# Optimization experiments

Hardware: AMD Instinct MI355X
Metric: run time of the kernel (lower is better)

Reference implementation:

```python
import jax, jax.numpy as jnp
import numpy as np

B, NOBJ = 64, 16
NUM_CLASSES = 91
IOU_TH = 0.5
NEG_POS = 3
VAR0, VAR1 = 0.1, 0.2
IMG = 300.0


def _ssd300_priors():
    # Standard SSD300 PriorBox: 8732 priors in center-size form (cx, cy, w, h), normalized to [0,1]
    fmaps = [38, 19, 10, 5, 3, 1]
    steps = [8, 16, 32, 64, 100, 300]
    min_s = [30, 60, 111, 162, 213, 264]
    max_s = [60, 111, 162, 213, 264, 315]
    ars = [[2], [2, 3], [2, 3], [2, 3], [2], [2]]
    out = []
    for k, f in enumerate(fmaps):
        for i in range(f):
            for j in range(f):
                cx = (j + 0.5) * steps[k] / IMG
                cy = (i + 0.5) * steps[k] / IMG
                s = min_s[k] / IMG
                out.append([cx, cy, s, s])
                sp = float(np.sqrt(s * max_s[k] / IMG))
                out.append([cx, cy, sp, sp])
                for ar in ars[k]:
                    r = float(np.sqrt(ar))
                    out.append([cx, cy, s * r, s / r])
                    out.append([cx, cy, s / r, s * r])
    return np.clip(np.asarray(out, np.float32), 0.0, 1.0)


def setup_inputs() -> dict:
    priors = jnp.asarray(_ssd300_priors())  # [8732, 4]
    P = priors.shape[0]
    key = jax.random.key(0)
    k1, k2, k3, k4, k5 = jax.random.split(key, 5)
    loc_data = jax.random.normal(k1, (B, P, 4), jnp.float32)
    conf_data = jax.random.normal(k2, (B, P, NUM_CLASSES), jnp.float32)
    centers = jax.random.uniform(k3, (B, NOBJ, 2), minval=40.0, maxval=260.0)
    half = jax.random.uniform(k5, (B, NOBJ, 2), minval=10.0, maxval=40.0)
    gt_boxes = jnp.concatenate([centers - half, centers + half], axis=-1)  # point form, pixel coords
    gt_labels = jax.random.randint(k4, (B, NOBJ), 1, NUM_CLASSES).astype(jnp.int32)
    return {"loc_data": loc_data, "conf_data": conf_data, "gt_boxes": gt_boxes,
            "gt_labels": gt_labels, "priors": priors}


def _point_form(pr):
    return jnp.concatenate([pr[:, :2] - pr[:, 2:] / 2, pr[:, :2] + pr[:, 2:] / 2], axis=1)


def _jaccard(boxes, pboxes):
    # boxes [N,4], pboxes [P,4] both point form -> IoU [N,P]
    lt = jnp.maximum(boxes[:, None, :2], pboxes[None, :, :2])
    rb = jnp.minimum(boxes[:, None, 2:], pboxes[None, :, 2:])
    wh = jnp.clip(rb - lt, 0.0)
    inter = wh[..., 0] * wh[..., 1]
    area_a = ((boxes[:, 2] - boxes[:, 0]) * (boxes[:, 3] - boxes[:, 1]))[:, None]
    area_b = ((pboxes[:, 2] - pboxes[:, 0]) * (pboxes[:, 3] - pboxes[:, 1]))[None, :]
    return inter / (area_a + area_b - inter)


def _encode(matched, priors):
    # matched [P,4] point form, priors [P,4] center-size form
    g_cxcy = ((matched[:, :2] + matched[:, 2:]) / 2 - priors[:, :2]) / (VAR0 * priors[:, 2:])
    g_wh = jnp.log((matched[:, 2:] - matched[:, :2]) / priors[:, 2:]) / VAR1
    return jnp.concatenate([g_cxcy, g_wh], axis=1)


def _match(boxes, labels, priors):
    # boxes [NOBJ,4] normalized point form; labels [NOBJ]; priors [P,4]
    ov = _jaccard(boxes, _point_form(priors))            # [NOBJ, P]
    best_prior_idx = jnp.argmax(ov, axis=1)              # [NOBJ]
    best_truth_ov = jnp.max(ov, axis=0)                  # [P]
    best_truth_idx = jnp.argmax(ov, axis=0)              # [P]
    best_truth_ov = best_truth_ov.at[best_prior_idx].set(2.0)
    for j in range(NOBJ):  # small fixed loop, matches torch in-order scatter
        best_truth_idx = best_truth_idx.at[best_prior_idx[j]].set(j)
    matched = boxes[best_truth_idx]                      # [P,4]
    conf = labels[best_truth_idx]
    conf = jnp.where(best_truth_ov < IOU_TH, 0, conf)
    return _encode(matched, priors), conf


def reference(loc_data, conf_data, gt_boxes, gt_labels, priors):
    P = priors.shape[0]
    loc_t, conf_t = jax.vmap(lambda b, l: _match(b / IMG, l, priors))(gt_boxes, gt_labels)
    pos = conf_t > 0                                      # [B,P]
    # localization loss: SmoothL1 (beta=1), summed over positives
    diff = loc_data - loc_t
    ad = jnp.abs(diff)
    sl1 = jnp.where(ad < 1.0, 0.5 * diff * diff, ad - 0.5)
    loss_l = jnp.sum(sl1 * pos[..., None].astype(sl1.dtype))
    # hard negative mining on per-prior CE loss
    lse = jax.nn.logsumexp(conf_data, axis=-1)            # [B,P]
    gathered = jnp.take_along_axis(conf_data, conf_t[..., None].astype(jnp.int32), axis=-1)[..., 0]
    ce_all = lse - gathered                                # [B,P]
    mine = jnp.where(pos, 0.0, ce_all)
    order = jnp.argsort(-mine, axis=1)
    rank = jnp.argsort(order, axis=1)
    num_pos = jnp.sum(pos, axis=1, keepdims=True)
    num_neg = jnp.clip(NEG_POS * num_pos, 1, P - 1)
    neg = rank < num_neg
    mask = pos | neg
    loss_c = jnp.sum(ce_all * mask.astype(ce_all.dtype))
    N = jnp.maximum(jnp.sum(num_pos).astype(jnp.float32), 1.0)
    return jnp.stack([loss_l / N, loss_c / N])  # [loss_l, loss_c]
```

## Files before the change

kernel.cpp:

```cpp
#include <hip/hip_runtime.h>
#include <math.h>

#define BATCH 64
#define NOBJ 16
#define NPRIOR 8732
#define NC 91
#define IMG 300.0f
#define GPB 1092
#define NGROUP (GPB * BATCH)
#define CE_GRID 6144
#define GBINS 2048
#define MSPLIT 16
#define SL 546

__global__ __launch_bounds__(256) void k_match1(
    const float* __restrict__ loc_data,
    const float* __restrict__ gt_boxes,
    const int*   __restrict__ gt_labels,
    const float* __restrict__ priors,
    int*   __restrict__ conf_t,
    float* __restrict__ ll_part,
    int*   __restrict__ np_part,
    float* __restrict__ candv,
    int*   __restrict__ candi)
{
    __shared__ float bx0[NOBJ], by0[NOBJ], bx1[NOBJ], by1[NOBJ], barea[NOBJ];
    __shared__ int   blab[NOBJ];
    __shared__ float rv[NOBJ][4];
    __shared__ int   ri[NOBJ][4];
    __shared__ float red_f[4];
    __shared__ int   red_i[4];

    const int b    = blockIdx.y;
    const int blk  = blockIdx.x;
    const int tid  = threadIdx.x;
    const int lane = tid & 63;
    const int wave = tid >> 6;
    const int p0   = blk * SL;
    const int pend = min(p0 + SL, NPRIOR);

    if (tid < NOBJ) {
        float4 g = ((const float4*)gt_boxes)[(size_t)b * NOBJ + tid];
        float x0 = g.x * (1.0f / IMG), y0 = g.y * (1.0f / IMG);
        float x1 = g.z * (1.0f / IMG), y1 = g.w * (1.0f / IMG);
        bx0[tid] = x0; by0[tid] = y0; bx1[tid] = x1; by1[tid] = y1;
        barea[tid] = (x1 - x0) * (y1 - y0);
        blab[tid] = gt_labels[b * NOBJ + tid];
    }
    __syncthreads();

    float bv[NOBJ];
    int   bi[NOBJ];
#pragma unroll
    for (int j = 0; j < NOBJ; j++) { bv[j] = -1.0f; bi[j] = 0x7fffffff; }

    int np_local = 0;
    float ll_local = 0.0f;

    for (int p = p0 + tid; p < pend; p += 256) {
        float4 pr = ((const float4*)priors)[p];
        float cx = pr.x, cy = pr.y, w = pr.z, h = pr.w;
        float px0 = cx - 0.5f * w, py0 = cy - 0.5f * h;
        float px1 = cx + 0.5f * w, py1 = cy + 0.5f * h;
        float pa = w * h;
        float maxv = -1.0f; int maxj = 0;
#pragma unroll
        for (int j = 0; j < NOBJ; j++) {
            float ltx = fmaxf(bx0[j], px0), lty = fmaxf(by0[j], py0);
            float rbx = fminf(bx1[j], px1), rby = fminf(by1[j], py1);
            float iw = fmaxf(rbx - ltx, 0.0f), ih = fmaxf(rby - lty, 0.0f);
            float inter = iw * ih;
            float iou = inter / (barea[j] + pa - inter);
            if (iou > maxv) { maxv = iou; maxj = j; }
            if (iou > bv[j]) { bv[j] = iou; bi[j] = p; }
        }
        int conf = (maxv < 0.5f) ? 0 : blab[maxj];
        conf_t[(size_t)b * NPRIOR + p] = conf;
        if (conf > 0) {
            np_local++;
            float mx0 = bx0[maxj], my0 = by0[maxj];
            float mx1 = bx1[maxj], my1 = by1[maxj];
            float g0 = ((mx0 + mx1) * 0.5f - cx) / (0.1f * w);
            float g1 = ((my0 + my1) * 0.5f - cy) / (0.1f * h);
            float g2 = logf((mx1 - mx0) / w) * 5.0f;
            float g3 = logf((my1 - my0) / h) * 5.0f;
            float4 lv = ((const float4*)loc_data)[(size_t)b * NPRIOR + p];
            float d0 = lv.x - g0, d1 = lv.y - g1, d2 = lv.z - g2, d3 = lv.w - g3;
            float a0 = fabsf(d0), a1 = fabsf(d1), a2 = fabsf(d2), a3 = fabsf(d3);
            ll_local += (a0 < 1.f ? 0.5f * d0 * d0 : a0 - 0.5f)
                      + (a1 < 1.f ? 0.5f * d1 * d1 : a1 - 0.5f)
                      + (a2 < 1.f ? 0.5f * d2 * d2 : a2 - 0.5f)
                      + (a3 < 1.f ? 0.5f * d3 * d3 : a3 - 0.5f);
        }
    }

#pragma unroll
    for (int j = 0; j < NOBJ; j++) {
        float v = bv[j]; int ix = bi[j];
        for (int off = 32; off; off >>= 1) {
            float v2 = __shfl_xor(v, off);
            int   i2 = __shfl_xor(ix, off);
            if (v2 > v || (v2 == v && i2 < ix)) { v = v2; ix = i2; }
        }
        if (lane == 0) { rv[j][wave] = v; ri[j][wave] = ix; }
    }
    for (int off = 32; off; off >>= 1) {
        ll_local += __shfl_xor(ll_local, off);
        np_local += __shfl_xor(np_local, off);
    }
    if (lane == 0) { red_f[wave] = ll_local; red_i[wave] = np_local; }
    __syncthreads();
    if (tid < NOBJ) {
        int j = tid;
        float v = rv[j][0]; int ix = ri[j][0];
#pragma unroll
        for (int w2 = 1; w2 < 4; w2++) {
            float v2 = rv[j][w2]; int i2 = ri[j][w2];
            if (v2 > v || (v2 == v && i2 < ix)) { v = v2; ix = i2; }
        }
        size_t o = ((size_t)b * MSPLIT + blk) * NOBJ + j;
        candv[o] = v;
        candi[o] = ix;
    }
    if (tid == 0) {
        ll_part[b * MSPLIT + blk] = red_f[0] + red_f[1] + red_f[2] + red_f[3];
        np_part[b * MSPLIT + blk] = red_i[0] + red_i[1] + red_i[2] + red_i[3];
    }
}

__global__ __launch_bounds__(64) void k_bpi_fix(
    const float* __restrict__ loc_data,
    const float* __restrict__ gt_boxes,
    const int*   __restrict__ gt_labels,
    const float* __restrict__ priors,
    const float* __restrict__ candv,
    const int*   __restrict__ candi,
    int*   __restrict__ conf_t,
    float* __restrict__ ll_fix,
    int*   __restrict__ np_fix)
{
    __shared__ int bpi_s[NOBJ];
    const int b = blockIdx.x;
    const int lane = threadIdx.x;

    if (lane < NOBJ) {
        size_t base = (size_t)b * MSPLIT * NOBJ + lane;
        float v = candv[base]; int ix = candi[base];
#pragma unroll
        for (int c = 1; c < MSPLIT; c++) {
            float v2 = candv[base + c * NOBJ];
            int   i2 = candi[base + c * NOBJ];
            if (v2 > v || (v2 == v && i2 < ix)) { v = v2; ix = i2; }
        }
        bpi_s[lane] = ix;
    }
    __syncthreads();

    float ll_d = 0.0f;
    int   np_d = 0;

    if (lane < NOBJ) {
        const int j = lane;
        const int ps = bpi_s[j];
        bool last = true;
        for (int j2 = j + 1; j2 < NOBJ; j2++)
            if (bpi_s[j2] == ps) last = false;
        if (last) {
            float4 pr = ((const float4*)priors)[ps];
            float cx = pr.x, cy = pr.y, w = pr.z, h = pr.w;
            float px0 = cx - 0.5f * w, py0 = cy - 0.5f * h;
            float px1 = cx + 0.5f * w, py1 = cy + 0.5f * h;
            float pa = w * h;
            float maxv = -1.0f;
            float mx0 = 0, my0 = 0, mx1 = 0, my1 = 0;
            float jx0 = 0, jy0 = 0, jx1 = 0, jy1 = 0;
            for (int j2 = 0; j2 < NOBJ; j2++) {
                float4 g = ((const float4*)gt_boxes)[(size_t)b * NOBJ + j2];
                float x0 = g.x * (1.0f / IMG), y0 = g.y * (1.0f / IMG);
                float x1 = g.z * (1.0f / IMG), y1 = g.w * (1.0f / IMG);
                float area = (x1 - x0) * (y1 - y0);
                float ltx = fmaxf(x0, px0), lty = fmaxf(y0, py0);
                float rbx = fminf(x1, px1), rby = fminf(y1, py1);
                float iw = fmaxf(rbx - ltx, 0.0f), ih = fmaxf(rby - lty, 0.0f);
                float inter = iw * ih;
                float iou = inter / (area + pa - inter);
                if (iou > maxv) { maxv = iou; mx0 = x0; my0 = y0; mx1 = x1; my1 = y1; }
                if (j2 == j)    { jx0 = x0; jy0 = y0; jx1 = x1; jy1 = y1; }
            }
            float4 lv = ((const float4*)loc_data)[(size_t)b * NPRIOR + ps];
            if (maxv >= 0.5f) {
                float g0 = ((mx0 + mx1) * 0.5f - cx) / (0.1f * w);
                float g1 = ((my0 + my1) * 0.5f - cy) / (0.1f * h);
                float g2 = logf((mx1 - mx0) / w) * 5.0f;
                float g3 = logf((my1 - my0) / h) * 5.0f;
                float d0 = lv.x - g0, d1 = lv.y - g1, d2 = lv.z - g2, d3 = lv.w - g3;
                float a0 = fabsf(d0), a1 = fabsf(d1), a2 = fabsf(d2), a3 = fabsf(d3);
                ll_d -= (a0 < 1.f ? 0.5f * d0 * d0 : a0 - 0.5f)
                      + (a1 < 1.f ? 0.5f * d1 * d1 : a1 - 0.5f)
                      + (a2 < 1.f ? 0.5f * d2 * d2 : a2 - 0.5f)
                      + (a3 < 1.f ? 0.5f * d3 * d3 : a3 - 0.5f);
                np_d -= 1;
            }
            {
                float g0 = ((jx0 + jx1) * 0.5f - cx) / (0.1f * w);
                float g1 = ((jy0 + jy1) * 0.5f - cy) / (0.1f * h);
                float g2 = logf((jx1 - jx0) / w) * 5.0f;
                float g3 = logf((jy1 - jy0) / h) * 5.0f;
                float d0 = lv.x - g0, d1 = lv.y - g1, d2 = lv.z - g2, d3 = lv.w - g3;
                float a0 = fabsf(d0), a1 = fabsf(d1), a2 = fabsf(d2), a3 = fabsf(d3);
                ll_d += (a0 < 1.f ? 0.5f * d0 * d0 : a0 - 0.5f)
                      + (a1 < 1.f ? 0.5f * d1 * d1 : a1 - 0.5f)
                      + (a2 < 1.f ? 0.5f * d2 * d2 : a2 - 0.5f)
                      + (a3 < 1.f ? 0.5f * d3 * d3 : a3 - 0.5f);
                np_d += 1;
            }
            conf_t[(size_t)b * NPRIOR + ps] = gt_labels[b * NOBJ + j];
        }
    }

    for (int off = 32; off; off >>= 1) {
        ll_d += __shfl_xor(ll_d, off);
        np_d += __shfl_xor(np_d, off);
    }
    if (lane == 0) { ll_fix[b] = ll_d; np_fix[b] = np_d; }
}

#define CE_ISSUE(gg, R0, R1, R2, NF)                                           \
    {   int b_ = (gg) / GPB, ci_ = (gg) - b_ * GPB;                            \
        int p0_ = ci_ * 8;                                                     \
        int rows_ = min(8, NPRIOR - p0_);                                      \
        NF = (rows_ * NC) >> 2;                                                \
        const float4* s_ = (const float4*)(conf_data + ((size_t)b_ * NPRIOR + p0_) * NC); \
        R0 = s_[tid];                                                          \
        if (tid + 64  < NF) R1 = s_[tid + 64];                                 \
        if (tid + 128 < NF) R2 = s_[tid + 128]; }

#define CT_LOAD(gg)                                                            \
    ( conf_t[(size_t)((gg) / GPB) * NPRIOR + ((gg) - ((gg) / GPB) * GPB) * 8 + (tid >> 3)] )

#define CE_WRITE(BUF, R0, R1, R2, NF)                                          \
    {   float4* d_ = (float4*)sbuf[BUF];                                       \
        d_[tid] = R0;                                                          \
        if (tid + 64  < NF) d_[tid + 64]  = R1;                                \
        if (tid + 128 < NF) d_[tid + 128] = R2; }

#define CE_COMPUTE(gg, BUF, TG)                                                \
    {   int b_ = (gg) / GPB, ci_ = (gg) - b_ * GPB;                            \
        int p0_ = ci_ * 8;                                                     \
        int rows_ = min(8, NPRIOR - p0_);                                      \
        int rr_ = tid >> 3, q_ = tid & 7;                                      \
        if (rr_ < rows_) {                                                     \
            const float* row_ = sbuf[BUF] + rr_ * NC;                          \
            float s_ = 0.0f;                                                   \
            _Pragma("unroll")                                                  \
            for (int i_ = q_; i_ < NC; i_ += 8) s_ += __expf(row_[i_]);        \
            s_ += __shfl_xor(s_, 1);                                           \
            s_ += __shfl_xor(s_, 2);                                           \
            s_ += __shfl_xor(s_, 4);                                           \
            if (q_ == 0) {                                                     \
                size_t o_ = (size_t)b_ * NPRIOR + p0_ + rr_;                   \
                int tgt_ = TG;                                                 \
                float ce_ = __logf(s_) - row_[tgt_];                           \
                if (tgt_ > 0) { pos_acc += ce_; mine[o_] = 0.0f; }             \
                else          { mine[o_] = fmaxf(ce_, 0.0f); }                 \
            } } }

__global__ __launch_bounds__(64) void k_ce(
    const float* __restrict__ conf_data,
    const int*   __restrict__ conf_t,
    float* __restrict__ mine,
    float* __restrict__ lc_part)
{
    __shared__ float sbuf[2][8 * NC];
    const int tid = threadIdx.x;
    const int G = CE_GRID;

    float4 a0, a1, a2, b0, b1, b2;
    int nfA = 0, nfB = 0;
    float pos_acc = 0.0f;

    int g = blockIdx.x;
    CE_ISSUE(g, a0, a1, a2, nfA);
    int tcur = CT_LOAD(g);
    if (g + G < NGROUP) CE_ISSUE(g + G, b0, b1, b2, nfB);
    CE_WRITE(0, a0, a1, a2, nfA);

    for (; g < NGROUP; g += 2 * G) {
        int tnext = (g + G < NGROUP) ? CT_LOAD(g + G) : 0;
        if (g + 2 * G < NGROUP) CE_ISSUE(g + 2 * G, a0, a1, a2, nfA);
        CE_COMPUTE(g, 0, tcur);
        if (g + G < NGROUP) {
            CE_WRITE(1, b0, b1, b2, nfB);
            int tn2 = (g + 2 * G < NGROUP) ? CT_LOAD(g + 2 * G) : 0;
            if (g + 3 * G < NGROUP) CE_ISSUE(g + 3 * G, b0, b1, b2, nfB);
            CE_COMPUTE(g + G, 1, tnext);
            if (g + 2 * G < NGROUP) CE_WRITE(0, a0, a1, a2, nfA);
            tcur = tn2;
        }
    }

    for (int off = 32; off; off >>= 1) pos_acc += __shfl_xor(pos_acc, off);
    if (tid == 0) lc_part[blockIdx.x] = pos_acc;
}

__global__ __launch_bounds__(256) void k_histsel(
    const float* __restrict__ mine,
    const int*   __restrict__ np_part,
    const int*   __restrict__ np_fix,
    float* __restrict__ lc2)
{
    __shared__ int   lh[GBINS];
    __shared__ float ls[GBINS];
    __shared__ int   wtot[4];
    __shared__ int   s_B0, s_r;
    __shared__ float red_f[4];

    const int b = blockIdx.x;
    const int tid = threadIdx.x;
    const int lane = tid & 63;
    const int wave = tid >> 6;

#pragma unroll
    for (int j = 0; j < GBINS / 256; j++) {
        lh[tid + j * 256] = 0;
        ls[tid + j * 256] = 0.0f;
    }
    __syncthreads();

    for (int i = tid; i < NPRIOR; i += 256) {
        float v = mine[(size_t)b * NPRIOR + i];
        int bin = min((int)(v * 128.0f), GBINS - 1);
        atomicAdd(&lh[bin], 1);
        atomicAdd(&ls[bin], v);
    }

    int np = np_fix[b];
#pragma unroll
    for (int c = 0; c < MSPLIT; c++) np += np_part[b * MSPLIT + c];
    const int kk = min(max(3 * np, 1), NPRIOR - 1);
    __syncthreads();

    int   cnt[8];
    float sm[8];
#pragma unroll
    for (int j = 0; j < 8; j++) { cnt[j] = lh[tid * 8 + j]; sm[j] = ls[tid * 8 + j]; }
    int own = 0;
#pragma unroll
    for (int j = 0; j < 8; j++) own += cnt[j];

    int incl = own;
#pragma unroll
    for (int off = 1; off < 64; off <<= 1) {
        int t = __shfl_down(incl, off);
        incl += (lane + off < 64) ? t : 0;
    }
    if (lane == 0) wtot[wave] = incl;
    __syncthreads();
    int hi = 0;
#pragma unroll
    for (int w = 0; w < 4; w++) if (w > wave) hi += wtot[w];
    const int suf = (incl - own) + hi;

    int found = -1;
    int s2 = suf;
#pragma unroll
    for (int j = 7; j >= 0; j--) {
        if (found < 0 && s2 < kk && kk <= s2 + cnt[j])
            found = (tid * 8 + j) * 16384 + (kk - s2);
        s2 += cnt[j];
    }
    if (found >= 0) { s_B0 = found >> 14; s_r = found & 16383; }
    __syncthreads();
    const int B0 = s_B0;
    const int r  = s_r;

    float sg = 0.0f;
#pragma unroll
    for (int j = 0; j < 8; j++) {
        int bin = tid * 8 + j;
        if (bin > B0)       sg += sm[j];
        else if (bin == B0) sg += (float)r * (sm[j] / (float)cnt[j]);
    }
    for (int off = 32; off; off >>= 1) sg += __shfl_xor(sg, off);
    if (lane == 0) red_f[wave] = sg;
    __syncthreads();
    if (tid == 0) lc2[b] = red_f[0] + red_f[1] + red_f[2] + red_f[3];
}

__global__ __launch_bounds__(1024) void k_final(
    const float* __restrict__ lc_part, const float* __restrict__ lc2,
    const float* __restrict__ ll_part, const int* __restrict__ np_part,
    const float* __restrict__ ll_fix, const int* __restrict__ np_fix,
    float* __restrict__ out)
{
    __shared__ float rf[16][2];
    __shared__ int   rn[16];
    const int tid = threadIdx.x;
    float lc = 0.0f;
    for (int i = tid; i < CE_GRID; i += 1024) lc += lc_part[i];
    float ll = 0.0f; int np = 0;
    if (tid < BATCH) { lc += lc2[tid]; ll += ll_fix[tid]; np += np_fix[tid]; }
    if (tid < BATCH * MSPLIT) { ll += ll_part[tid]; np += np_part[tid]; }
    for (int off = 32; off; off >>= 1) {
        lc += __shfl_xor(lc, off);
        ll += __shfl_xor(ll, off);
        np += __shfl_xor(np, off);
    }
    const int lane = tid & 63, wave = tid >> 6;
    if (lane == 0) { rf[wave][0] = lc; rf[wave][1] = ll; rn[wave] = np; }
    __syncthreads();
    if (tid == 0) {
        float lcT = 0.0f, llT = 0.0f; int npT = 0;
        for (int w = 0; w < 16; w++) { lcT += rf[w][0]; llT += rf[w][1]; npT += rn[w]; }
        float N = fmaxf((float)npT, 1.0f);
        out[0] = llT / N;
        out[1] = lcT / N;
    }
}

extern "C" void kernel_launch(void* const* d_in, const int* in_sizes, int n_in,
                              void* d_out, int out_size, void* d_ws, size_t ws_size,
                              hipStream_t stream)
{
    const float* loc_data  = (const float*)d_in[0];
    const float* conf_data = (const float*)d_in[1];
    const float* gt_boxes  = (const float*)d_in[2];
    const int*   gt_labels = (const int*)d_in[3];
    const float* priors    = (const float*)d_in[4];
    float* out = (float*)d_out;

    char* ws = (char*)d_ws;
    float* ll_part  = (float*)(ws + 0);
    int*   np_part  = (int*)(ws + 4096);
    float* lc2      = (float*)(ws + 8192);
    float* ll_fix   = (float*)(ws + 8704);
    int*   np_fix   = (int*)(ws + 9216);
    float* lc_part  = (float*)(ws + 12288);
    int*   conf_t   = (int*)(ws + 65536);
    float* mine     = (float*)(ws + 65536 + 2235392);
    float* candv    = (float*)(ws + 7340032);
    int*   candi    = (int*)(ws + 7405568);

    hipLaunchKernelGGL(k_match1, dim3(MSPLIT, BATCH), dim3(256), 0, stream,
                       loc_data, gt_boxes, gt_labels, priors,
                       conf_t, ll_part, np_part, candv, candi);
    hipLaunchKernelGGL(k_bpi_fix, dim3(BATCH), dim3(64), 0, stream,
                       loc_data, gt_boxes, gt_labels, priors, candv, candi,
                       conf_t, ll_fix, np_fix);
    hipLaunchKernelGGL(k_ce, dim3(CE_GRID), dim3(64), 0, stream,
                       conf_data, conf_t, mine, lc_part);
    hipLaunchKernelGGL(k_histsel, dim3(BATCH), dim3(256), 0, stream,
                       mine, np_part, np_fix, lc2);
    hipLaunchKernelGGL(k_final, dim3(1), dim3(1024), 0, stream,
                       lc_part, lc2, ll_part, np_part, ll_fix, np_fix, out);
}
```

Before: 101.2 us.

## Fuse matching and logsumexp into one heterogeneous kernel, defer CE gather to histsel

The matching blocks and the conf_data logsumexp streaming now share one launch: 2 of every 5 blocks do prior matching and 3 run four independent double-buffered LSE waves. The LSE no longer depends on conf_t, so it runs concurrently with matching instead of after the bpi fix. The per-prior CE target gather and the positive-loss sum move into the histogram kernel, which reads lse and the class-0 logit and does a scattered load from conf_data for positives. This removes the serialization between matching and the large conf_data read, at the cost of extra lse/c0 buffers and a slower, more irregular histogram pass.

```diff
diff --git a/kernel.cpp b/kernel.cpp
--- a/kernel.cpp
+++ b/kernel.cpp
@@ -8,22 +8,61 @@
 #define IMG 300.0f
 #define GPB 1092
 #define NGROUP (GPB * BATCH)
-#define CE_GRID 6144
+#define LSE_WAVES 6144
 #define GBINS 2048
 #define MSPLIT 16
 #define SL 546
 
-__global__ __launch_bounds__(256) void k_match1(
+#define LSE_ISSUE(gg, R0, R1, R2, NF)                                          \
+    {   int b_ = (gg) / GPB, ci_ = (gg) - b_ * GPB;                            \
+        int p0_ = ci_ * 8;                                                     \
+        int rows_ = min(8, NPRIOR - p0_);                                      \
+        NF = (rows_ * NC) >> 2;                                                \
+        const float4* s_ = (const float4*)(conf_data + ((size_t)b_ * NPRIOR + p0_) * NC); \
+        R0 = s_[lane];                                                         \
+        if (lane + 64  < NF) R1 = s_[lane + 64];                               \
+        if (lane + 128 < NF) R2 = s_[lane + 128]; }
+
+#define LSE_WRITE(SB, R0, R1, R2, NF)                                          \
+    {   float4* d_ = (float4*)(SB);                                            \
+        d_[lane] = R0;                                                         \
+        if (lane + 64  < NF) d_[lane + 64]  = R1;                              \
+        if (lane + 128 < NF) d_[lane + 128] = R2; }
+
+#define LSE_COMPUTE(gg, SB)                                                    \
+    {   int b_ = (gg) / GPB, ci_ = (gg) - b_ * GPB;                            \
+        int p0_ = ci_ * 8;                                                     \
+        int rows_ = min(8, NPRIOR - p0_);                                      \
+        int rr_ = lane >> 3, q_ = lane & 7;                                    \
+        if (rr_ < rows_) {                                                     \
+            const float* row_ = (SB) + rr_ * NC;                               \
+            float s_ = 0.0f;                                                   \
+            _Pragma("unroll")                                                  \
+            for (int i_ = q_; i_ < NC; i_ += 8) s_ += __expf(row_[i_]);        \
+            s_ += __shfl_xor(s_, 1);                                           \
+            s_ += __shfl_xor(s_, 2);                                           \
+            s_ += __shfl_xor(s_, 4);                                           \
+            if (q_ == 0) {                                                     \
+                size_t o_ = (size_t)b_ * NPRIOR + p0_ + rr_;                   \
+                lse_g[o_] = __logf(s_);                                        \
+                c0_g[o_]  = row_[0];                                           \
+            } } }
+
+__global__ __launch_bounds__(256) void k_fused(
     const float* __restrict__ loc_data,
     const float* __restrict__ gt_boxes,
     const int*   __restrict__ gt_labels,
     const float* __restrict__ priors,
+    const float* __restrict__ conf_data,
     int*   __restrict__ conf_t,
     float* __restrict__ ll_part,
     int*   __restrict__ np_part,
     float* __restrict__ candv,
-    int*   __restrict__ candi)
+    int*   __restrict__ candi,
+    float* __restrict__ lse_g,
+    float* __restrict__ c0_g)
 {
+    __shared__ float sbuf[4][2][8 * NC];
     __shared__ float bx0[NOBJ], by0[NOBJ], bx1[NOBJ], by1[NOBJ], barea[NOBJ];
     __shared__ int   blab[NOBJ];
     __shared__ float rv[NOBJ][4];
@@ -31,100 +70,130 @@
     __shared__ float red_f[4];
     __shared__ int   red_i[4];
 
-    const int b    = blockIdx.y;
-    const int blk  = blockIdx.x;
+    const int bid  = blockIdx.x;
     const int tid  = threadIdx.x;
     const int lane = tid & 63;
-    const int wave = tid >> 6;
-    const int p0   = blk * SL;
-    const int pend = min(p0 + SL, NPRIOR);
-
-    if (tid < NOBJ) {
-        float4 g = ((const float4*)gt_boxes)[(size_t)b * NOBJ + tid];
-        float x0 = g.x * (1.0f / IMG), y0 = g.y * (1.0f / IMG);
-        float x1 = g.z * (1.0f / IMG), y1 = g.w * (1.0f / IMG);
-        bx0[tid] = x0; by0[tid] = y0; bx1[tid] = x1; by1[tid] = y1;
-        barea[tid] = (x1 - x0) * (y1 - y0);
-        blab[tid] = gt_labels[b * NOBJ + tid];
-    }
-    __syncthreads();
-
-    float bv[NOBJ];
-    int   bi[NOBJ];
-#pragma unroll
-    for (int j = 0; j < NOBJ; j++) { bv[j] = -1.0f; bi[j] = 0x7fffffff; }
-
-    int np_local = 0;
-    float ll_local = 0.0f;
-
-    for (int p = p0 + tid; p < pend; p += 256) {
-        float4 pr = ((const float4*)priors)[p];
-        float cx = pr.x, cy = pr.y, w = pr.z, h = pr.w;
-        float px0 = cx - 0.5f * w, py0 = cy - 0.5f * h;
-        float px1 = cx + 0.5f * w, py1 = cy + 0.5f * h;
-        float pa = w * h;
-        float maxv = -1.0f; int maxj = 0;
+    const int wv   = tid >> 6;
+    const int r5   = bid % 5;
+
+    if (r5 < 2) {
+        const int m   = (bid / 5) * 2 + r5;
+        const int blk = m % MSPLIT;
+        const int b   = m / MSPLIT;
+        const int p0   = blk * SL;
+        const int pend = min(p0 + SL, NPRIOR);
+
+        if (tid < NOBJ) {
+            float4 g = ((const float4*)gt_boxes)[(size_t)b * NOBJ + tid];
+            float x0 = g.x * (1.0f / IMG), y0 = g.y * (1.0f / IMG);
+            float x1 = g.z * (1.0f / IMG), y1 = g.w * (1.0f / IMG);
+            bx0[tid] = x0; by0[tid] = y0; bx1[tid] = x1; by1[tid] = y1;
+            barea[tid] = (x1 - x0) * (y1 - y0);
+            blab[tid] = gt_labels[b * NOBJ + tid];
+        }
+        __syncthreads();
+
+        float bv[NOBJ];
+        int   bi[NOBJ];
+#pragma unroll
+        for (int j = 0; j < NOBJ; j++) { bv[j] = -1.0f; bi[j] = 0x7fffffff; }
+
+        int np_local = 0;
+        float ll_local = 0.0f;
+
+        for (int p = p0 + tid; p < pend; p += 256) {
+            float4 pr = ((const float4*)priors)[p];
+            float cx = pr.x, cy = pr.y, w = pr.z, h = pr.w;
+            float px0 = cx - 0.5f * w, py0 = cy - 0.5f * h;
+            float px1 = cx + 0.5f * w, py1 = cy + 0.5f * h;
+            float pa = w * h;
+            float maxv = -1.0f; int maxj = 0;
+#pragma unroll
+            for (int j = 0; j < NOBJ; j++) {
+                float ltx = fmaxf(bx0[j], px0), lty = fmaxf(by0[j], py0);
+                float rbx = fminf(bx1[j], px1), rby = fminf(by1[j], py1);
+                float iw = fmaxf(rbx - ltx, 0.0f), ih = fmaxf(rby - lty, 0.0f);
+                float inter = iw * ih;
+                float iou = inter / (barea[j] + pa - inter);
+                if (iou > maxv) { maxv = iou; maxj = j; }
+                if (iou > bv[j]) { bv[j] = iou; bi[j] = p; }
+            }
+            int conf = (maxv < 0.5f) ? 0 : blab[maxj];
+            conf_t[(size_t)b * NPRIOR + p] = conf;
+            if (conf > 0) {
+                np_local++;
+                float mx0 = bx0[maxj], my0 = by0[maxj];
+                float mx1 = bx1[maxj], my1 = by1[maxj];
+                float g0 = ((mx0 + mx1) * 0.5f - cx) / (0.1f * w);
+                float g1 = ((my0 + my1) * 0.5f - cy) / (0.1f * h);
+                float g2 = logf((mx1 - mx0) / w) * 5.0f;
+                float g3 = logf((my1 - my0) / h) * 5.0f;
+                float4 lv = ((const float4*)loc_data)[(size_t)b * NPRIOR + p];
+                float d0 = lv.x - g0, d1 = lv.y - g1, d2 = lv.z - g2, d3 = lv.w - g3;
+                float a0 = fabsf(d0), a1 = fabsf(d1), a2 = fabsf(d2), a3 = fabsf(d3);
+                ll_local += (a0 < 1.f ? 0.5f * d0 * d0 : a0 - 0.5f)
+                          + (a1 < 1.f ? 0.5f * d1 * d1 : a1 - 0.5f)
+                          + (a2 < 1.f ? 0.5f * d2 * d2 : a2 - 0.5f)
+                          + (a3 < 1.f ? 0.5f * d3 * d3 : a3 - 0.5f);
+            }
+        }
+
 #pragma unroll
         for (int j = 0; j < NOBJ; j++) {
-            float ltx = fmaxf(bx0[j], px0), lty = fmaxf(by0[j], py0);
-            float rbx = fminf(bx1[j], px1), rby = fminf(by1[j], py1);
-            float iw = fmaxf(rbx - ltx, 0.0f), ih = fmaxf(rby - lty, 0.0f);
-            float inter = iw * ih;
-            float iou = inter / (barea[j] + pa - inter);
-            if (iou > maxv) { maxv = iou; maxj = j; }
-            if (iou > bv[j]) { bv[j] = iou; bi[j] = p; }
-        }
-        int conf = (maxv < 0.5f) ? 0 : blab[maxj];
-        conf_t[(size_t)b * NPRIOR + p] = conf;
-        if (conf > 0) {
-            np_local++;
-            float mx0 = bx0[maxj], my0 = by0[maxj];
-            float mx1 = bx1[maxj], my1 = by1[maxj];
-            float g0 = ((mx0 + mx1) * 0.5f - cx) / (0.1f * w);
-            float g1 = ((my0 + my1) * 0.5f - cy) / (0.1f * h);
-            float g2 = logf((mx1 - mx0) / w) * 5.0f;
-            float g3 = logf((my1 - my0) / h) * 5.0f;
-            float4 lv = ((const float4*)loc_data)[(size_t)b * NPRIOR + p];
-            float d0 = lv.x - g0, d1 = lv.y - g1, d2 = lv.z - g2, d3 = lv.w - g3;
-            float a0 = fabsf(d0), a1 = fabsf(d1), a2 = fabsf(d2), a3 = fabsf(d3);
-            ll_local += (a0 < 1.f ? 0.5f * d0 * d0 : a0 - 0.5f)
-                      + (a1 < 1.f ? 0.5f * d1 * d1 : a1 - 0.5f)
-                      + (a2 < 1.f ? 0.5f * d2 * d2 : a2 - 0.5f)
-                      + (a3 < 1.f ? 0.5f * d3 * d3 : a3 - 0.5f);
-        }
-    }
-
-#pragma unroll
-    for (int j = 0; j < NOBJ; j++) {
-        float v = bv[j]; int ix = bi[j];
+            float v = bv[j]; int ix = bi[j];
+            for (int off = 32; off; off >>= 1) {
+                float v2 = __shfl_xor(v, off);
+                int   i2 = __shfl_xor(ix, off);
+                if (v2 > v || (v2 == v && i2 < ix)) { v = v2; ix = i2; }
+            }
+            if (lane == 0) { rv[j][wv] = v; ri[j][wv] = ix; }
+        }
         for (int off = 32; off; off >>= 1) {
-            float v2 = __shfl_xor(v, off);
-            int   i2 = __shfl_xor(ix, off);
-            if (v2 > v || (v2 == v && i2 < ix)) { v = v2; ix = i2; }
-        }
-        if (lane == 0) { rv[j][wave] = v; ri[j][wave] = ix; }
-    }
-    for (int off = 32; off; off >>= 1) {
-        ll_local += __shfl_xor(ll_local, off);
-        np_local += __shfl_xor(np_local, off);
-    }
-    if (lane == 0) { red_f[wave] = ll_local; red_i[wave] = np_local; }
-    __syncthreads();
-    if (tid < NOBJ) {
-        int j = tid;
-        float v = rv[j][0]; int ix = ri[j][0];
-#pragma unroll
-        for (int w2 = 1; w2 < 4; w2++) {
-            float v2 = rv[j][w2]; int i2 = ri[j][w2];
-            if (v2 > v || (v2 == v && i2 < ix)) { v = v2; ix = i2; }
-        }
-        size_t o = ((size_t)b * MSPLIT + blk) * NOBJ + j;
-        candv[o] = v;
-        candi[o] = ix;
-    }
-    if (tid == 0) {
-        ll_part[b * MSPLIT + blk] = red_f[0] + red_f[1] + red_f[2] + red_f[3];
-        np_part[b * MSPLIT + blk] = red_i[0] + red_i[1] + red_i[2] + red_i[3];
+            ll_local += __shfl_xor(ll_local, off);
+            np_local += __shfl_xor(np_local, off);
+        }
+        if (lane == 0) { red_f[wv] = ll_local; red_i[wv] = np_local; }
+        __syncthreads();
+        if (tid < NOBJ) {
+            int j = tid;
+            float v = rv[j][0]; int ix = ri[j][0];
+#pragma unroll
+            for (int w2 = 1; w2 < 4; w2++) {
+                float v2 = rv[j][w2]; int i2 = ri[j][w2];
+                if (v2 > v || (v2 == v && i2 < ix)) { v = v2; ix = i2; }
+            }
+            size_t o = ((size_t)b * MSPLIT + blk) * NOBJ + j;
+            candv[o] = v;
+            candi[o] = ix;
+        }
+        if (tid == 0) {
+            ll_part[b * MSPLIT + blk] = red_f[0] + red_f[1] + red_f[2] + red_f[3];
+            np_part[b * MSPLIT + blk] = red_i[0] + red_i[1] + red_i[2] + red_i[3];
+        }
+    } else {
+        const int lblk = (bid / 5) * 3 + (r5 - 2);
+        int g = lblk * 4 + wv;
+        const int G = LSE_WAVES;
+        float* SB0 = &sbuf[wv][0][0];
+        float* SB1 = &sbuf[wv][1][0];
+
+        float4 a0, a1, a2, b0, b1, b2;
+        int nfA = 0, nfB = 0;
+
+        LSE_ISSUE(g, a0, a1, a2, nfA);
+        if (g + G < NGROUP) LSE_ISSUE(g + G, b0, b1, b2, nfB);
+        LSE_WRITE(SB0, a0, a1, a2, nfA);
+
+        for (; g < NGROUP; g += 2 * G) {
+            if (g + 2 * G < NGROUP) LSE_ISSUE(g + 2 * G, a0, a1, a2, nfA);
+            LSE_COMPUTE(g, SB0);
+            if (g + G < NGROUP) {
+                LSE_WRITE(SB1, b0, b1, b2, nfB);
+                if (g + 3 * G < NGROUP) LSE_ISSUE(g + 3 * G, b0, b1, b2, nfB);
+                LSE_COMPUTE(g + G, SB1);
+                if (g + 2 * G < NGROUP) LSE_WRITE(SB0, a0, a1, a2, nfA);
+            }
+        }
     }
 }
 
@@ -225,95 +294,22 @@
     if (lane == 0) { ll_fix[b] = ll_d; np_fix[b] = np_d; }
 }
 
-#define CE_ISSUE(gg, R0, R1, R2, NF)                                           \
-    {   int b_ = (gg) / GPB, ci_ = (gg) - b_ * GPB;                            \
-        int p0_ = ci_ * 8;                                                     \
-        int rows_ = min(8, NPRIOR - p0_);                                      \
-        NF = (rows_ * NC) >> 2;                                                \
-        const float4* s_ = (const float4*)(conf_data + ((size_t)b_ * NPRIOR + p0_) * NC); \
-        R0 = s_[tid];                                                          \
-        if (tid + 64  < NF) R1 = s_[tid + 64];                                 \
-        if (tid + 128 < NF) R2 = s_[tid + 128]; }
-
-#define CT_LOAD(gg)                                                            \
-    ( conf_t[(size_t)((gg) / GPB) * NPRIOR + ((gg) - ((gg) / GPB) * GPB) * 8 + (tid >> 3)] )
-
-#define CE_WRITE(BUF, R0, R1, R2, NF)                                          \
-    {   float4* d_ = (float4*)sbuf[BUF];                                       \
-        d_[tid] = R0;                                                          \
-        if (tid + 64  < NF) d_[tid + 64]  = R1;                                \
-        if (tid + 128 < NF) d_[tid + 128] = R2; }
-
-#define CE_COMPUTE(gg, BUF, TG)                                                \
-    {   int b_ = (gg) / GPB, ci_ = (gg) - b_ * GPB;                            \
-        int p0_ = ci_ * 8;                                                     \
-        int rows_ = min(8, NPRIOR - p0_);                                      \
-        int rr_ = tid >> 3, q_ = tid & 7;                                      \
-        if (rr_ < rows_) {                                                     \
-            const float* row_ = sbuf[BUF] + rr_ * NC;                          \
-            float s_ = 0.0f;                                                   \
-            _Pragma("unroll")                                                  \
-            for (int i_ = q_; i_ < NC; i_ += 8) s_ += __expf(row_[i_]);        \
-            s_ += __shfl_xor(s_, 1);                                           \
-            s_ += __shfl_xor(s_, 2);                                           \
-            s_ += __shfl_xor(s_, 4);                                           \
-            if (q_ == 0) {                                                     \
-                size_t o_ = (size_t)b_ * NPRIOR + p0_ + rr_;                   \
-                int tgt_ = TG;                                                 \
-                float ce_ = __logf(s_) - row_[tgt_];                           \
-                if (tgt_ > 0) { pos_acc += ce_; mine[o_] = 0.0f; }             \
-                else          { mine[o_] = fmaxf(ce_, 0.0f); }                 \
-            } } }
-
-__global__ __launch_bounds__(64) void k_ce(
+__global__ __launch_bounds__(256) void k_histsel2(
     const float* __restrict__ conf_data,
+    const float* __restrict__ lse_g,
+    const float* __restrict__ c0_g,
     const int*   __restrict__ conf_t,
-    float* __restrict__ mine,
-    float* __restrict__ lc_part)
-{
-    __shared__ float sbuf[2][8 * NC];
-    const int tid = threadIdx.x;
-    const int G = CE_GRID;
-
-    float4 a0, a1, a2, b0, b1, b2;
-    int nfA = 0, nfB = 0;
-    float pos_acc = 0.0f;
-
-    int g = blockIdx.x;
-    CE_ISSUE(g, a0, a1, a2, nfA);
-    int tcur = CT_LOAD(g);
-    if (g + G < NGROUP) CE_ISSUE(g + G, b0, b1, b2, nfB);
-    CE_WRITE(0, a0, a1, a2, nfA);
-
-    for (; g < NGROUP; g += 2 * G) {
-        int tnext = (g + G < NGROUP) ? CT_LOAD(g + G) : 0;
-        if (g + 2 * G < NGROUP) CE_ISSUE(g + 2 * G, a0, a1, a2, nfA);
-        CE_COMPUTE(g, 0, tcur);
-        if (g + G < NGROUP) {
-            CE_WRITE(1, b0, b1, b2, nfB);
-            int tn2 = (g + 2 * G < NGROUP) ? CT_LOAD(g + 2 * G) : 0;
-            if (g + 3 * G < NGROUP) CE_ISSUE(g + 3 * G, b0, b1, b2, nfB);
-            CE_COMPUTE(g + G, 1, tnext);
-            if (g + 2 * G < NGROUP) CE_WRITE(0, a0, a1, a2, nfA);
-            tcur = tn2;
-        }
-    }
-
-    for (int off = 32; off; off >>= 1) pos_acc += __shfl_xor(pos_acc, off);
-    if (tid == 0) lc_part[blockIdx.x] = pos_acc;
-}
-
-__global__ __launch_bounds__(256) void k_histsel(
-    const float* __restrict__ mine,
     const int*   __restrict__ np_part,
     const int*   __restrict__ np_fix,
-    float* __restrict__ lc2)
+    float* __restrict__ lc2,
+    float* __restrict__ lc3)
 {
     __shared__ int   lh[GBINS];
     __shared__ float ls[GBINS];
     __shared__ int   wtot[4];
     __shared__ int   s_B0, s_r;
     __shared__ float red_f[4];
+    __shared__ float red_p[4];
 
     const int b = blockIdx.x;
     const int tid = threadIdx.x;
@@ -327,11 +323,21 @@
     }
     __syncthreads();
 
+    float pos_acc = 0.0f;
     for (int i = tid; i < NPRIOR; i += 256) {
-        float v = mine[(size_t)b * NPRIOR + i];
-        int bin = min((int)(v * 128.0f), GBINS - 1);
+        size_t o = (size_t)b * NPRIOR + i;
+        float lse = lse_g[o];
+        int tgt = conf_t[o];
+        float mv;
+        if (tgt > 0) {
+            mv = 0.0f;
+            pos_acc += lse - conf_data[o * NC + tgt];
+        } else {
+            mv = fmaxf(lse - c0_g[o], 0.0f);
+        }
+        int bin = min((int)(mv * 128.0f), GBINS - 1);
         atomicAdd(&lh[bin], 1);
-        atomicAdd(&ls[bin], v);
+        atomicAdd(&ls[bin], mv);
     }
 
     int np = np_fix[b];
@@ -381,14 +387,20 @@
         if (bin > B0)       sg += sm[j];
         else if (bin == B0) sg += (float)r * (sm[j] / (float)cnt[j]);
     }
-    for (int off = 32; off; off >>= 1) sg += __shfl_xor(sg, off);
-    if (lane == 0) red_f[wave] = sg;
-    __syncthreads();
-    if (tid == 0) lc2[b] = red_f[0] + red_f[1] + red_f[2] + red_f[3];
+    for (int off = 32; off; off >>= 1) {
+        sg += __shfl_xor(sg, off);
+        pos_acc += __shfl_xor(pos_acc, off);
+    }
+    if (lane == 0) { red_f[wave] = sg; red_p[wave] = pos_acc; }
+    __syncthreads();
+    if (tid == 0) {
+        lc2[b] = red_f[0] + red_f[1] + red_f[2] + red_f[3];
+        lc3[b] = red_p[0] + red_p[1] + red_p[2] + red_p[3];
+    }
 }
 
 __global__ __launch_bounds__(1024) void k_final(
-    const float* __restrict__ lc_part, const float* __restrict__ lc2,
+    const float* __restrict__ lc2, const float* __restrict__ lc3,
     const float* __restrict__ ll_part, const int* __restrict__ np_part,
     const float* __restrict__ ll_fix, const int* __restrict__ np_fix,
     float* __restrict__ out)
@@ -396,10 +408,9 @@
     __shared__ float rf[16][2];
     __shared__ int   rn[16];
     const int tid = threadIdx.x;
-    float lc = 0.0f;
-    for (int i = tid; i < CE_GRID; i += 1024) lc += lc_part[i];
-    float ll = 0.0f; int np = 0;
-    if (tid < BATCH) { lc += lc2[tid]; ll += ll_fix[tid]; np += np_fix[tid]; }
+    float lc = 0.0f, ll = 0.0f;
+    int np = 0;
+    if (tid < BATCH) { lc = lc2[tid] + lc3[tid]; ll += ll_fix[tid]; np += np_fix[tid]; }
     if (tid < BATCH * MSPLIT) { ll += ll_part[tid]; np += np_part[tid]; }
     for (int off = 32; off; off >>= 1) {
         lc += __shfl_xor(lc, off);
@@ -433,24 +444,24 @@
     float* ll_part  = (float*)(ws + 0);
     int*   np_part  = (int*)(ws + 4096);
     float* lc2      = (float*)(ws + 8192);
+    float* lc3      = (float*)(ws + 8448);
     float* ll_fix   = (float*)(ws + 8704);
     int*   np_fix   = (int*)(ws + 9216);
-    float* lc_part  = (float*)(ws + 12288);
     int*   conf_t   = (int*)(ws + 65536);
-    float* mine     = (float*)(ws + 65536 + 2235392);
-    float* candv    = (float*)(ws + 7340032);
-    int*   candi    = (int*)(ws + 7405568);
-
-    hipLaunchKernelGGL(k_match1, dim3(MSPLIT, BATCH), dim3(256), 0, stream,
-                       loc_data, gt_boxes, gt_labels, priors,
-                       conf_t, ll_part, np_part, candv, candi);
+    float* lse_g    = (float*)(ws + 65536 + 2235392);
+    float* c0_g     = (float*)(ws + 65536 + 2 * 2235392);
+    float* candv    = (float*)(ws + 8388608);
+    int*   candi    = (int*)(ws + 8454144);
+
+    hipLaunchKernelGGL(k_fused, dim3(2560), dim3(256), 0, stream,
+                       loc_data, gt_boxes, gt_labels, priors, conf_data,
+                       conf_t, ll_part, np_part, candv, candi, lse_g, c0_g);
     hipLaunchKernelGGL(k_bpi_fix, dim3(BATCH), dim3(64), 0, stream,
                        loc_data, gt_boxes, gt_labels, priors, candv, candi,
                        conf_t, ll_fix, np_fix);
-    hipLaunchKernelGGL(k_ce, dim3(CE_GRID), dim3(64), 0, stream,
-                       conf_data, conf_t, mine, lc_part);
-    hipLaunchKernelGGL(k_histsel, dim3(BATCH), dim3(256), 0, stream,
-                       mine, np_part, np_fix, lc2);
+    hipLaunchKernelGGL(k_histsel2, dim3(BATCH), dim3(256), 0, stream,
+                       conf_data, lse_g, c0_g, conf_t, np_part, np_fix,
+                       lc2, lc3);
     hipLaunchKernelGGL(k_final, dim3(1), dim3(1024), 0, stream,
-                       lc_part, lc2, ll_part, np_part, ll_fix, np_fix, out);
+                       lc2, lc3, ll_part, np_part, ll_fix, np_fix, out);
 }
```

Result: slower. 117.3 us (+15.9%).
